# Kernel optimization log

Measured on AMD Instinct MI355X. Metric: run time of the kernel, lower is better.

The kernel has to match this reference:

```python
import jax, jax.numpy as jnp
import numpy as np

B, S, D = 4, 2048, 1024
NUM_HEADS = 16
KQ = D // NUM_HEADS  # 64


def setup_inputs() -> dict:
    key = jax.random.key(0)
    ks = jax.random.split(key, 4)
    # he_uniform fan_in = D: limit = sqrt(6/fan_in)
    lim = np.sqrt(6.0 / D).astype(np.float32)
    x = jax.random.normal(ks[0], (B, S, D), dtype=jnp.float32)
    Wq = jax.random.uniform(ks[1], (D, KQ), minval=-lim, maxval=lim, dtype=jnp.float32)
    Wk = jax.random.uniform(ks[2], (D, KQ), minval=-lim, maxval=lim, dtype=jnp.float32)
    Wv = jax.random.uniform(ks[3], (D, KQ), minval=-lim, maxval=lim, dtype=jnp.float32)
    Bq = jnp.zeros((S, KQ), dtype=jnp.float32)
    Bk = jnp.zeros((S, KQ), dtype=jnp.float32)
    Bv = jnp.zeros((S, KQ), dtype=jnp.float32)
    return {"x": x, "Wq": Wq, "Bq": Bq, "Wk": Wk, "Bk": Bk, "Wv": Wv, "Bv": Bv}


def reference(x, Wq, Bq, Wk, Bk, Wv, Bv):
    # Q/K/V: [B,S,KQ]; biases are per-position [S,KQ], broadcast over batch
    Q = jnp.einsum('bsd,dk->bsk', x, Wq) + Bq
    K = jnp.einsum('bsd,dk->bsk', x, Wk) + Bk
    V = jnp.einsum('bsd,dk->bsk', x, Wv) + Bv
    scale = 1.0 / jnp.sqrt(jnp.float32(KQ))
    scores = jnp.einsum('bqk,bsk->bqs', Q, K) * scale  # [B,S,S]
    attn = jax.nn.softmax(scores, axis=-1)
    return jnp.einsum('bqs,bsk->bqk', attn, V)  # [B,S,KQ]
```

## Files before the change

### kernel.cpp

```cpp
#include <hip/hip_runtime.h>
#include <stdint.h>

#define NBATCH 4
#define NS 2048
#define ND 1024
#define NK 64
#define QSCALE 0.18033688011112042f

typedef __attribute__((ext_vector_type(4))) float f32x4;
typedef __attribute__((ext_vector_type(16))) float f32x16;
typedef __attribute__((ext_vector_type(8))) short bf16x8;
typedef unsigned short u16;
typedef unsigned int u32;
typedef unsigned long long u64;

__device__ __forceinline__ u16 f2bf(float f) {
  union { float f; u32 u; } v; v.f = f;
  u32 u = v.u;
  u += 0x7FFFu + ((u >> 16) & 1u);
  return (u16)(u >> 16);
}

__device__ __forceinline__ u32 pk2(float lo, float hi) {
  u32 r;
  asm("v_cvt_pk_bf16_f32 %0, %1, %2" : "=v"(r) : "v"(lo), "v"(hi));
  return r;
}

__device__ __forceinline__ void gll16(const void* g, void* l) {
  __builtin_amdgcn_global_load_lds(
      (const __attribute__((address_space(1))) unsigned int*)g,
      (__attribute__((address_space(3))) unsigned int*)l, 16, 0, 0);
}

__global__ __launch_bounds__(256) void wtrans_kernel(
    const float* __restrict__ Wq, const float* __restrict__ Wk,
    const float* __restrict__ Wv, u16* __restrict__ Wt) {
  __shared__ float tile[64][65];
  int blk = blockIdx.x;
  int m = blk >> 4, dt = blk & 15;
  const float* W = (m == 0) ? Wq : (m == 1) ? Wk : Wv;
  int d0 = dt * 64;
  int t = threadIdx.x;
#pragma unroll
  for (int i = 0; i < 16; i++) {
    int idx = t + 256 * i;
    int dd = idx >> 6, c = idx & 63;
    tile[dd][c] = W[(d0 + dd) * 64 + c];
  }
  __syncthreads();
#pragma unroll
  for (int i = 0; i < 16; i++) {
    int idx = t + 256 * i;
    int c = idx >> 6, dd = idx & 63;
    Wt[(m * 64 + c) * 1024 + d0 + dd] = f2bf(tile[dd][c]);
  }
}

__global__ __launch_bounds__(512) void qkv_kernel(
    const float* __restrict__ x, const u16* __restrict__ Wt,
    const float* __restrict__ Bq, const float* __restrict__ Bk,
    const float* __restrict__ Bv, u16* __restrict__ Qf,
    u16* __restrict__ Kf, u16* __restrict__ Vf) {
  __shared__ __attribute__((aligned(16))) char lds[98304];
  char* ldsx = lds;
  char* ldsw = lds + 24576;

  int tid = threadIdx.x;
  int w = tid >> 6, lane = tid & 63;
  int g = lane >> 4, c = lane & 15;
  int rh = w & 1, cq = w >> 1;

  int xrow_l = 4 * w + (lane >> 4);
  long xrow_g = (long)blockIdx.x * 32 + xrow_l;
  int xs32 = ((lane >> 1) & 7) ^ (xrow_l & 7);
  const char* xg = (const char*)(x + xrow_g * ND) + xs32 * 32 + (lane & 1) * 16;

  int wr0 = 8 * w + (lane >> 3);
  const char* wg0 = (const char*)(Wt + (long)(wr0)       * ND) + (((lane & 7) ^ (wr0 & 7)) * 16);
  const char* wg1 = (const char*)(Wt + (long)(64 + wr0)  * ND) + (((lane & 7) ^ (wr0 & 7)) * 16);
  const char* wg2 = (const char*)(Wt + (long)(128 + wr0) * ND) + (((lane & 7) ^ (wr0 & 7)) * 16);
  int wd0 = (8 * w) * 128, wd1 = (64 + 8 * w) * 128, wd2 = (128 + 8 * w) * 128;

  int rowa = rh * 16 + c;
  int axor = rowa & 7;
  int aoff0 = rowa * 256 + ((g ^ axor) * 32);
  int aoff1 = rowa * 256 + (((4 + g) ^ axor) * 32);
  int boff[3][2];
#pragma unroll
  for (int tt = 0; tt < 3; tt++) {
    int col = cq * 48 + tt * 16 + c;
#pragma unroll
    for (int kk = 0; kk < 2; kk++)
      boff[tt][kk] = col * 128 + (((kk * 4 + g) ^ (col & 7)) * 16);
  }

  f32x4 acc[3];
#pragma unroll
  for (int tt = 0; tt < 3; tt++) acc[tt] = (f32x4){0.f, 0.f, 0.f, 0.f};

#define STAGE(BUF, T) do {                                            \
    gll16(xg + (long)(T) * 256, ldsx + (BUF) * 8192 + w * 1024);      \
    gll16(wg0 + (T) * 128, ldsw + (BUF) * 24576 + wd0);               \
    gll16(wg1 + (T) * 128, ldsw + (BUF) * 24576 + wd1);               \
    gll16(wg2 + (T) * 128, ldsw + (BUF) * 24576 + wd2);               \
  } while (0)

#define COMPUTE(B) do {                                               \
    const char* xb_ = ldsx + (B) * 8192;                              \
    const char* wb_ = ldsw + (B) * 24576;                             \
    f32x4 p0_ = *(const f32x4*)(xb_ + aoff0);                         \
    f32x4 p1_ = *(const f32x4*)(xb_ + aoff0 + 16);                    \
    f32x4 p2_ = *(const f32x4*)(xb_ + aoff1);                         \
    f32x4 p3_ = *(const f32x4*)(xb_ + aoff1 + 16);                    \
    union { bf16x8 v; u32 w[4]; } af0, af1;                           \
    af0.w[0] = pk2(p0_[0], p0_[1]); af0.w[1] = pk2(p0_[2], p0_[3]);   \
    af0.w[2] = pk2(p1_[0], p1_[1]); af0.w[3] = pk2(p1_[2], p1_[3]);   \
    af1.w[0] = pk2(p2_[0], p2_[1]); af1.w[1] = pk2(p2_[2], p2_[3]);   \
    af1.w[2] = pk2(p3_[0], p3_[1]); af1.w[3] = pk2(p3_[2], p3_[3]);   \
    _Pragma("unroll")                                                 \
    for (int tt = 0; tt < 3; tt++) {                                  \
      bf16x8 b0_ = *(const bf16x8*)(wb_ + boff[tt][0]);               \
      bf16x8 b1_ = *(const bf16x8*)(wb_ + boff[tt][1]);               \
      acc[tt] = __builtin_amdgcn_mfma_f32_16x16x32_bf16(af0.v, b0_, acc[tt], 0, 0, 0); \
      acc[tt] = __builtin_amdgcn_mfma_f32_16x16x32_bf16(af1.v, b1_, acc[tt], 0, 0, 0); \
    }                                                                 \
  } while (0)

  STAGE(0, 0);
  STAGE(1, 1);
#pragma unroll
  for (int t = 0; t < 16; t++) {
    if (t < 15) asm volatile("s_waitcnt vmcnt(4)" ::: "memory");
    else        asm volatile("s_waitcnt vmcnt(0)" ::: "memory");
    __builtin_amdgcn_s_barrier();
    __builtin_amdgcn_sched_barrier(0);
    if (t + 2 < 16) STAGE((t + 2) % 3, t + 2);
    __builtin_amdgcn_sched_barrier(0);
    COMPUTE(t % 3);
  }
#undef STAGE
#undef COMPUTE

  __syncthreads();
  u16* ep = (u16*)lds;
  int il = blockIdx.x & 63, bb = blockIdx.x >> 6;
#pragma unroll
  for (int tt = 0; tt < 3; tt++) {
    int colg = cq * 48 + tt * 16 + c;
    int mtx = colg >> 6;
    int col = colg & 63;
    const float* Bias = (mtx == 0) ? Bq : (mtx == 1) ? Bk : Bv;
#pragma unroll
    for (int j = 0; j < 4; j++) {
      int sl = rh * 16 + 4 * g + j;
      float v = acc[tt][j] + Bias[(il * 32 + sl) * NK + col];
      if (mtx == 0) v *= QSCALE;
      int chunk, off;
      if (mtx < 2) {
        chunk = mtx * 4 + (col >> 4);
        off = (sl + ((col >> 3) & 1) * 32) * 8 + (col & 7);
      } else {
        chunk = 8 + (col >> 5) * 2 + (sl >> 4);
        off = ((col & 31) + ((sl >> 3) & 1) * 32) * 8 + (sl & 7);
      }
      ep[chunk * 512 + off] = f2bf(v);
    }
  }
  __syncthreads();
  for (int t5 = tid; t5 < 768; t5 += 512) {
    int ch = t5 >> 6, pc = t5 & 63;
    bf16x8 val = *(const bf16x8*)(ep + ch * 512 + pc * 8);
    u16* dst;
    if (ch < 4)
      dst = Qf + (((long)bb * 64 + il) * 4 + ch) * 512 + pc * 8;
    else if (ch < 8)
      dst = Kf + (((long)bb * 64 + il) * 4 + (ch - 4)) * 512 + pc * 8;
    else {
      int half = (ch - 8) >> 1, iv = (ch - 8) & 1;
      dst = Vf + ((((long)bb * 2 + half) * 32 + (il >> 1)) * 4 + 2 * (il & 1) + iv) * 512 + pc * 8;
    }
    *(bf16x8*)dst = val;
  }
}

__device__ __forceinline__ bf16x8 pack8(float p0, float p1, float p2, float p3,
                                        float p4, float p5, float p6, float p7,
                                        int hi) {
  u32 A = pk2(p0, p1), B = pk2(p2, p3), C = pk2(p4, p5), D = pk2(p6, p7);
  u32 sA = (u32)__shfl_xor((int)A, 32);
  u32 sB = (u32)__shfl_xor((int)B, 32);
  u32 sC = (u32)__shfl_xor((int)C, 32);
  u32 sD = (u32)__shfl_xor((int)D, 32);
  union { u32 w[4]; bf16x8 v; } u;
  u.w[0] = hi ? sC : A;
  u.w[1] = hi ? sD : B;
  u.w[2] = hi ? C : sA;
  u.w[3] = hi ? D : sB;
  return u.v;
}

__global__ __launch_bounds__(256) __attribute__((amdgpu_waves_per_eu(2, 2)))
void attn_kernel(
    const u16* __restrict__ Qf, const u16* __restrict__ Kf,
    const u16* __restrict__ Vf, float* __restrict__ Opart,
    float* __restrict__ lpart) {
  __shared__ float Ol[4][32][64];
  __shared__ float Ll[4][32];
  int w = threadIdx.x >> 6, lane = threadIdx.x & 63;
  int q = lane & 31, hi = lane >> 5;
  int bid = blockIdx.x;
  int b = (bid & 7) >> 1;
  int half = (bid >> 3) & 1;
  int qt = ((bid >> 4) << 1) | (bid & 1);
  long qglob = (long)b * NS + qt * 32;

  bf16x8 qf[4];
  {
    const u16* qp = Qf + ((long)b * 64 + qt) * 2048 + lane * 8;
#pragma unroll
    for (int kk = 0; kk < 4; kk++) qf[kk] = *(const bf16x8*)(qp + kk * 512);
  }
  const u16* kcp = Kf + ((long)b * 64 + half * 32 + w * 8) * 2048 + lane * 8;
  const u16* vcp0 = Vf + ((long)(b * 2) * 32 + half * 16 + w * 4) * 2048 + lane * 8;
  const u16* vcp1 = Vf + ((long)(b * 2 + 1) * 32 + half * 16 + w * 4) * 2048 + lane * 8;

  f32x16 o0, o1;
#pragma unroll
  for (int r = 0; r < 16; r++) { o0[r] = 0.f; o1[r] = 0.f; }
  float lacc[4] = {0.f, 0.f, 0.f, 0.f};

  bf16x8 kA0[4], kA1[4], kB0[4], kB1[4];
#pragma unroll
  for (int kk = 0; kk < 4; kk++) {
    kA0[kk] = *(const bf16x8*)(kcp + kk * 512);
    kA1[kk] = *(const bf16x8*)(kcp + 2048 + kk * 512);
  }

#define ATTN_STEP(T, KC0, KC1, KN0, KN1)                                      \
  do {                                                                        \
    int t_ = (T);                                                             \
    bf16x8 vf0[4], vf1[4];                                                    \
    _Pragma("unroll") for (int i = 0; i < 4; i++) {                           \
      vf0[i] = *(const bf16x8*)(vcp0 + t_ * 2048 + i * 512);                  \
      vf1[i] = *(const bf16x8*)(vcp1 + t_ * 2048 + i * 512);                  \
    }                                                                         \
    if (t_ + 1 < 4) {                                                         \
      const u16* kn_ = kcp + (long)(t_ + 1) * 4096;                           \
      _Pragma("unroll") for (int i = 0; i < 4; i++) {                         \
        KN0[i] = *(const bf16x8*)(kn_ + i * 512);                             \
        KN1[i] = *(const bf16x8*)(kn_ + 2048 + i * 512);                      \
      }                                                                       \
    }                                                                         \
    __builtin_amdgcn_sched_barrier(0);                                        \
    f32x16 s0, s1;                                                            \
    _Pragma("unroll") for (int r = 0; r < 16; r++) { s0[r] = 0.f; s1[r] = 0.f; } \
    _Pragma("unroll") for (int i = 0; i < 4; i++)                             \
      s0 = __builtin_amdgcn_mfma_f32_32x32x16_bf16(KC0[i], qf[i], s0, 0, 0, 0); \
    _Pragma("unroll") for (int i = 0; i < 4; i++)                             \
      s1 = __builtin_amdgcn_mfma_f32_32x32x16_bf16(KC1[i], qf[i], s1, 0, 0, 0); \
    _Pragma("unroll") for (int r = 0; r < 16; r++) {                          \
      s0[r] = exp2f(s0[r]); s1[r] = exp2f(s1[r]);                             \
      lacc[r & 3] += s0[r] + s1[r];                                           \
    }                                                                         \
    bf16x8 pa[4];                                                             \
    pa[0] = pack8(s0[0], s0[1], s0[2], s0[3], s0[4], s0[5], s0[6], s0[7], hi);   \
    pa[1] = pack8(s0[8], s0[9], s0[10], s0[11], s0[12], s0[13], s0[14], s0[15], hi); \
    pa[2] = pack8(s1[0], s1[1], s1[2], s1[3], s1[4], s1[5], s1[6], s1[7], hi);   \
    pa[3] = pack8(s1[8], s1[9], s1[10], s1[11], s1[12], s1[13], s1[14], s1[15], hi); \
    _Pragma("unroll") for (int i = 0; i < 4; i++) {                           \
      o0 = __builtin_amdgcn_mfma_f32_32x32x16_bf16(pa[i], vf0[i], o0, 0, 0, 0); \
      o1 = __builtin_amdgcn_mfma_f32_32x32x16_bf16(pa[i], vf1[i], o1, 0, 0, 0); \
    }                                                                         \
  } while (0)

  ATTN_STEP(0, kA0, kA1, kB0, kB1);
  ATTN_STEP(1, kB0, kB1, kA0, kA1);
  ATTN_STEP(2, kA0, kA1, kB0, kB1);
  ATTN_STEP(3, kB0, kB1, kA0, kA1);
#undef ATTN_STEP

  float lt = (lacc[0] + lacc[1]) + (lacc[2] + lacc[3]);
  lt += __shfl_xor(lt, 32);

#pragma unroll
  for (int r = 0; r < 16; r++) {
    int qq = (r & 3) + 8 * (r >> 2) + 4 * hi;
    Ol[w][qq][q]      = o0[r];
    Ol[w][qq][q + 32] = o1[r];
  }
  if (hi == 0) Ll[w][q] = lt;
  __syncthreads();

#pragma unroll
  for (int rr = 2; rr >= 1; rr >>= 1) {
    if (w < rr) {
#pragma unroll
      for (int i = 0; i < 8; i++) {
        int idx = lane + i * 64;
        f32x4* dst = (f32x4*)&Ol[w][idx >> 4][(idx & 15) * 4];
        const f32x4* src = (const f32x4*)&Ol[w + rr][idx >> 4][(idx & 15) * 4];
        *dst += *src;
      }
      if (lane < 32) Ll[w][lane] += Ll[w + rr][lane];
    }
    __syncthreads();
  }

  long ob = (long)half * (NBATCH * NS * NK);
#pragma unroll
  for (int ii = 0; ii < 2; ii++) {
    int idx = threadIdx.x + ii * 256;
    int row = idx >> 4, c4 = (idx & 15) * 4;
    f32x4 v = *(const f32x4*)&Ol[0][row][c4];
    *(f32x4*)&Opart[ob + (qglob + row) * NK + c4] = v;
  }
  if (threadIdx.x < 32)
    lpart[half * (NBATCH * NS) + qglob + threadIdx.x] = Ll[0][threadIdx.x];
}

__global__ __launch_bounds__(256) void combine_kernel(
    const float* __restrict__ Opart, const float* __restrict__ lpart,
    float* __restrict__ out, int nsplit) {
  int gid = blockIdx.x * 256 + threadIdx.x;
  int rw = gid >> 4, c4 = (gid & 15) * 4;
  f32x4 a = (f32x4){0.f, 0.f, 0.f, 0.f};
  float l = 0.f;
  for (int sp = 0; sp < nsplit; sp++) {
    a += *(const f32x4*)(Opart + (long)sp * (NBATCH * NS * NK) + (long)rw * NK + c4);
    l += lpart[sp * (NBATCH * NS) + rw];
  }
  float inv = 1.0f / l;
  f32x4 r;
#pragma unroll
  for (int i = 0; i < 4; i++) r[i] = a[i] * inv;
  *(f32x4*)(out + (long)rw * NK + c4) = r;
}

extern "C" void kernel_launch(void* const* d_in, const int* in_sizes, int n_in,
                              void* d_out, int out_size, void* d_ws, size_t ws_size,
                              hipStream_t stream) {
  const float* x  = (const float*)d_in[0];
  const float* Wq = (const float*)d_in[1];
  const float* Bq = (const float*)d_in[2];
  const float* Wk = (const float*)d_in[3];
  const float* Bk = (const float*)d_in[4];
  const float* Wv = (const float*)d_in[5];
  const float* Bv = (const float*)d_in[6];
  float* out = (float*)d_out;

  char* ws = (char*)d_ws;
  u16* Wt = (u16*)ws;
  u16* Qf = (u16*)(ws + 393216);
  u16* Kf = (u16*)(ws + 1441792);
  u16* Vf = (u16*)(ws + 2490368);
  float* lpart = (float*)(ws + 3538944);
  float* Opart = (float*)(ws + 3801088);

  wtrans_kernel<<<dim3(48), dim3(256), 0, stream>>>(Wq, Wk, Wv, Wt);
  qkv_kernel<<<dim3(256), dim3(512), 0, stream>>>(x, Wt, Bq, Bk, Bv, Qf, Kf, Vf);
  attn_kernel<<<dim3(512), dim3(256), 0, stream>>>(Qf, Kf, Vf, Opart, lpart);
  combine_kernel<<<dim3(512), dim3(256), 0, stream>>>(Opart, lpart, out, 2);
}
```

Baseline: 34.67 us.

## Stage shared K/V chunk in LDS and split keys eight ways across blocks

The attention kernel changes from 4 waves splitting one query tile's keys and reducing through LDS to 8 waves each owning a different query tile. All 8 waves share a 256-key K/V chunk that is cooperatively loaded into 64KB of LDS. The key split grows from 2 to 8, so each wave writes its partial output straight to global memory with nontemporal stores and the combine kernel sums 8 partials. This removes the intra-block LDS reduction and reuses K/V across query tiles, but it adds more partial-output traffic and loses the register double-buffering of K/V loads.

```diff
diff --git a/kernel.cpp b/kernel.cpp
--- a/kernel.cpp
+++ b/kernel.cpp
@@ -200,123 +200,101 @@
   return u.v;
 }
 
-__global__ __launch_bounds__(256) __attribute__((amdgpu_waves_per_eu(2, 2)))
+__global__ __launch_bounds__(512) __attribute__((amdgpu_waves_per_eu(2, 2)))
 void attn_kernel(
     const u16* __restrict__ Qf, const u16* __restrict__ Kf,
     const u16* __restrict__ Vf, float* __restrict__ Opart,
     float* __restrict__ lpart) {
-  __shared__ float Ol[4][32][64];
-  __shared__ float Ll[4][32];
-  int w = threadIdx.x >> 6, lane = threadIdx.x & 63;
+  __shared__ __attribute__((aligned(16))) char kv[65536];
+  int tid = threadIdx.x;
+  int w = tid >> 6, lane = tid & 63;
   int q = lane & 31, hi = lane >> 5;
   int bid = blockIdx.x;
-  int b = (bid & 7) >> 1;
-  int half = (bid >> 3) & 1;
-  int qt = ((bid >> 4) << 1) | (bid & 1);
+  int b = bid >> 6, sp = (bid >> 3) & 7, qg = bid & 7;
+  int qt = qg * 8 + w;
   long qglob = (long)b * NS + qt * 32;
+
+  {
+    const u16* ksrc = Kf + ((long)b * 64 + sp * 8) * 2048;
+    const u16* v0src = Vf + ((long)(b * 2) * 32 + sp * 4) * 2048;
+    const u16* v1src = Vf + ((long)(b * 2 + 1) * 32 + sp * 4) * 2048;
+#pragma unroll
+    for (int i = 0; i < 8; i++) {
+      int idx = tid + i * 512;
+      const u16* src = (idx < 2048) ? ksrc + idx * 8
+                     : (idx < 3072) ? v0src + (idx - 2048) * 8
+                                    : v1src + (idx - 3072) * 8;
+      *(bf16x8*)(kv + idx * 16) = *(const bf16x8*)src;
+    }
+  }
 
   bf16x8 qf[4];
   {
     const u16* qp = Qf + ((long)b * 64 + qt) * 2048 + lane * 8;
 #pragma unroll
-    for (int kk = 0; kk < 4; kk++) qf[kk] = *(const bf16x8*)(qp + kk * 512);
-  }
-  const u16* kcp = Kf + ((long)b * 64 + half * 32 + w * 8) * 2048 + lane * 8;
-  const u16* vcp0 = Vf + ((long)(b * 2) * 32 + half * 16 + w * 4) * 2048 + lane * 8;
-  const u16* vcp1 = Vf + ((long)(b * 2 + 1) * 32 + half * 16 + w * 4) * 2048 + lane * 8;
+    for (int kk = 0; kk < 4; kk++)
+      qf[kk] = __builtin_nontemporal_load((const bf16x8*)(qp + kk * 512));
+  }
 
   f32x16 o0, o1;
 #pragma unroll
   for (int r = 0; r < 16; r++) { o0[r] = 0.f; o1[r] = 0.f; }
   float lacc[4] = {0.f, 0.f, 0.f, 0.f};
 
-  bf16x8 kA0[4], kA1[4], kB0[4], kB1[4];
-#pragma unroll
-  for (int kk = 0; kk < 4; kk++) {
-    kA0[kk] = *(const bf16x8*)(kcp + kk * 512);
-    kA1[kk] = *(const bf16x8*)(kcp + 2048 + kk * 512);
-  }
-
-#define ATTN_STEP(T, KC0, KC1, KN0, KN1)                                      \
-  do {                                                                        \
-    int t_ = (T);                                                             \
-    bf16x8 vf0[4], vf1[4];                                                    \
-    _Pragma("unroll") for (int i = 0; i < 4; i++) {                           \
-      vf0[i] = *(const bf16x8*)(vcp0 + t_ * 2048 + i * 512);                  \
-      vf1[i] = *(const bf16x8*)(vcp1 + t_ * 2048 + i * 512);                  \
-    }                                                                         \
-    if (t_ + 1 < 4) {                                                         \
-      const u16* kn_ = kcp + (long)(t_ + 1) * 4096;                           \
-      _Pragma("unroll") for (int i = 0; i < 4; i++) {                         \
-        KN0[i] = *(const bf16x8*)(kn_ + i * 512);                             \
-        KN1[i] = *(const bf16x8*)(kn_ + 2048 + i * 512);                      \
-      }                                                                       \
-    }                                                                         \
-    __builtin_amdgcn_sched_barrier(0);                                        \
-    f32x16 s0, s1;                                                            \
-    _Pragma("unroll") for (int r = 0; r < 16; r++) { s0[r] = 0.f; s1[r] = 0.f; } \
-    _Pragma("unroll") for (int i = 0; i < 4; i++)                             \
-      s0 = __builtin_amdgcn_mfma_f32_32x32x16_bf16(KC0[i], qf[i], s0, 0, 0, 0); \
-    _Pragma("unroll") for (int i = 0; i < 4; i++)                             \
-      s1 = __builtin_amdgcn_mfma_f32_32x32x16_bf16(KC1[i], qf[i], s1, 0, 0, 0); \
-    _Pragma("unroll") for (int r = 0; r < 16; r++) {                          \
-      s0[r] = exp2f(s0[r]); s1[r] = exp2f(s1[r]);                             \
-      lacc[r & 3] += s0[r] + s1[r];                                           \
-    }                                                                         \
-    bf16x8 pa[4];                                                             \
-    pa[0] = pack8(s0[0], s0[1], s0[2], s0[3], s0[4], s0[5], s0[6], s0[7], hi);   \
-    pa[1] = pack8(s0[8], s0[9], s0[10], s0[11], s0[12], s0[13], s0[14], s0[15], hi); \
-    pa[2] = pack8(s1[0], s1[1], s1[2], s1[3], s1[4], s1[5], s1[6], s1[7], hi);   \
-    pa[3] = pack8(s1[8], s1[9], s1[10], s1[11], s1[12], s1[13], s1[14], s1[15], hi); \
-    _Pragma("unroll") for (int i = 0; i < 4; i++) {                           \
-      o0 = __builtin_amdgcn_mfma_f32_32x32x16_bf16(pa[i], vf0[i], o0, 0, 0, 0); \
-      o1 = __builtin_amdgcn_mfma_f32_32x32x16_bf16(pa[i], vf1[i], o1, 0, 0, 0); \
-    }                                                                         \
-  } while (0)
-
-  ATTN_STEP(0, kA0, kA1, kB0, kB1);
-  ATTN_STEP(1, kB0, kB1, kA0, kA1);
-  ATTN_STEP(2, kA0, kA1, kB0, kB1);
-  ATTN_STEP(3, kB0, kB1, kA0, kA1);
-#undef ATTN_STEP
+  __syncthreads();
+
+  const char* Kl = kv;
+  const char* V0 = kv + 32768;
+  const char* V1 = kv + 49152;
+
+#pragma unroll
+  for (int t = 0; t < 4; t++) {
+    bf16x8 kf0[4], kf1[4], vf0[4], vf1[4];
+#pragma unroll
+    for (int i = 0; i < 4; i++) {
+      kf0[i] = *(const bf16x8*)(Kl + ((t * 2) * 4 + i) * 1024 + lane * 16);
+      kf1[i] = *(const bf16x8*)(Kl + ((t * 2 + 1) * 4 + i) * 1024 + lane * 16);
+      vf0[i] = *(const bf16x8*)(V0 + (t * 4 + i) * 1024 + lane * 16);
+      vf1[i] = *(const bf16x8*)(V1 + (t * 4 + i) * 1024 + lane * 16);
+    }
+    f32x16 s0, s1;
+#pragma unroll
+    for (int r = 0; r < 16; r++) { s0[r] = 0.f; s1[r] = 0.f; }
+#pragma unroll
+    for (int i = 0; i < 4; i++)
+      s0 = __builtin_amdgcn_mfma_f32_32x32x16_bf16(kf0[i], qf[i], s0, 0, 0, 0);
+#pragma unroll
+    for (int i = 0; i < 4; i++)
+      s1 = __builtin_amdgcn_mfma_f32_32x32x16_bf16(kf1[i], qf[i], s1, 0, 0, 0);
+#pragma unroll
+    for (int r = 0; r < 16; r++) {
+      s0[r] = exp2f(s0[r]); s1[r] = exp2f(s1[r]);
+      lacc[r & 3] += s0[r] + s1[r];
+    }
+    bf16x8 pa[4];
+    pa[0] = pack8(s0[0], s0[1], s0[2], s0[3], s0[4], s0[5], s0[6], s0[7], hi);
+    pa[1] = pack8(s0[8], s0[9], s0[10], s0[11], s0[12], s0[13], s0[14], s0[15], hi);
+    pa[2] = pack8(s1[0], s1[1], s1[2], s1[3], s1[4], s1[5], s1[6], s1[7], hi);
+    pa[3] = pack8(s1[8], s1[9], s1[10], s1[11], s1[12], s1[13], s1[14], s1[15], hi);
+#pragma unroll
+    for (int i = 0; i < 4; i++) {
+      o0 = __builtin_amdgcn_mfma_f32_32x32x16_bf16(pa[i], vf0[i], o0, 0, 0, 0);
+      o1 = __builtin_amdgcn_mfma_f32_32x32x16_bf16(pa[i], vf1[i], o1, 0, 0, 0);
+    }
+  }
 
   float lt = (lacc[0] + lacc[1]) + (lacc[2] + lacc[3]);
   lt += __shfl_xor(lt, 32);
 
+  long ob = (long)sp * (NBATCH * NS * NK);
 #pragma unroll
   for (int r = 0; r < 16; r++) {
     int qq = (r & 3) + 8 * (r >> 2) + 4 * hi;
-    Ol[w][qq][q]      = o0[r];
-    Ol[w][qq][q + 32] = o1[r];
-  }
-  if (hi == 0) Ll[w][q] = lt;
-  __syncthreads();
-
-#pragma unroll
-  for (int rr = 2; rr >= 1; rr >>= 1) {
-    if (w < rr) {
-#pragma unroll
-      for (int i = 0; i < 8; i++) {
-        int idx = lane + i * 64;
-        f32x4* dst = (f32x4*)&Ol[w][idx >> 4][(idx & 15) * 4];
-        const f32x4* src = (const f32x4*)&Ol[w + rr][idx >> 4][(idx & 15) * 4];
-        *dst += *src;
-      }
-      if (lane < 32) Ll[w][lane] += Ll[w + rr][lane];
-    }
-    __syncthreads();
-  }
-
-  long ob = (long)half * (NBATCH * NS * NK);
-#pragma unroll
-  for (int ii = 0; ii < 2; ii++) {
-    int idx = threadIdx.x + ii * 256;
-    int row = idx >> 4, c4 = (idx & 15) * 4;
-    f32x4 v = *(const f32x4*)&Ol[0][row][c4];
-    *(f32x4*)&Opart[ob + (qglob + row) * NK + c4] = v;
-  }
-  if (threadIdx.x < 32)
-    lpart[half * (NBATCH * NS) + qglob + threadIdx.x] = Ll[0][threadIdx.x];
+    float* op = Opart + ob + (qglob + qq) * NK + q;
+    __builtin_nontemporal_store(o0[r], op);
+    __builtin_nontemporal_store(o1[r], op + 32);
+  }
+  if (hi == 0) lpart[sp * (NBATCH * NS) + qglob + q] = lt;
 }
 
 __global__ __launch_bounds__(256) void combine_kernel(
@@ -359,6 +337,6 @@
 
   wtrans_kernel<<<dim3(48), dim3(256), 0, stream>>>(Wq, Wk, Wv, Wt);
   qkv_kernel<<<dim3(256), dim3(512), 0, stream>>>(x, Wt, Bq, Bk, Bv, Qf, Kf, Vf);
-  attn_kernel<<<dim3(512), dim3(256), 0, stream>>>(Qf, Kf, Vf, Opart, lpart);
-  combine_kernel<<<dim3(512), dim3(256), 0, stream>>>(Opart, lpart, out, 2);
-}
+  attn_kernel<<<dim3(256), dim3(512), 0, stream>>>(Qf, Kf, Vf, Opart, lpart);
+  combine_kernel<<<dim3(512), dim3(256), 0, stream>>>(Opart, lpart, out, 8);
+}
```

Measured after the change: 38.33 us. 1.11x slower.
